# Kernel optimization log

Measured on AMD Instinct MI355X. Metric: run time of the kernel, lower is better.

Reference implementation:

```python
import jax, jax.numpy as jnp
import numpy as np

H = 4096
V = 32000
IGNORE_INDEX = -100
BETA = 0.1
ALPHA = 1.0
LABEL_SMOOTHING = 0.0


def setup_inputs() -> dict:
    key = jax.random.key(0)
    k1, k2, k3 = jax.random.split(key, 3)
    # (2B, T, H): first half chosen, second half rejected
    x = jax.random.normal(k1, (8, 512, H), dtype=jnp.float32)
    y = jax.random.randint(k2, (8, 512), 0, V)
    # LM-head weight, torch Linear layout (V, H)
    W = jax.random.normal(k3, (V, H), dtype=jnp.float32) * 0.02
    return {"x": x, "y": y, "W": W}


def reference(x, y, W):
    # Fused linear + CPO preference loss (math of LigerFusedLinearCPOLoss).
    # logits: (2B, T, V)
    logits = jnp.einsum("bth,vh->btv", x, W)
    logp = jax.nn.log_softmax(logits, axis=-1)

    loss_mask = (y != IGNORE_INDEX)
    y_safe = jnp.where(loss_mask, y, 0)
    # per-token target log-prob: (2B, T)
    tok_lp = jnp.take_along_axis(logp, y_safe[..., None], axis=-1)[..., 0]
    maskf = loss_mask.astype(logp.dtype)

    # per-sequence average log-prob over non-ignored tokens: (2B,)
    avg_lp = (tok_lp * maskf).sum(-1) / maskf.sum(-1)

    B2 = x.shape[0]
    B = B2 // 2
    chosen_logps = avg_lp[:B]
    rejected_logps = avg_lp[B:]

    # CPO preference term (simple sigmoid loss with label smoothing)
    d = BETA * (chosen_logps - rejected_logps)
    pref_loss = (
        -jax.nn.log_sigmoid(d) * (1.0 - LABEL_SMOOTHING)
        - jax.nn.log_sigmoid(-d) * LABEL_SMOOTHING
    ).sum() / B

    # NLL term on the chosen half, normalized by chosen non-ignored token count
    nll = -(tok_lp[:B] * maskf[:B]).sum() / maskf[:B].sum()

    return ALPHA * nll + pref_loss
```

## Files before the change

kernel.cpp:

```cpp
#include <hip/hip_runtime.h>
#include <hip/hip_bf16.h>

#define H_DIM 4096
#define M_TOK 4096
#define V_DIM 32000
#define BM 128
#define BN 128
#define BK 64

typedef unsigned short ushort_t;
typedef __attribute__((ext_vector_type(8))) short short8;
typedef __attribute__((ext_vector_type(4))) float f32x4;

__device__ __forceinline__ unsigned short f2bf(float f) {
    unsigned int u = __float_as_uint(f);
    u += 0x7FFFu + ((u >> 16) & 1u);
    return (unsigned short)(u >> 16);
}

__device__ __forceinline__ void gl2lds16(const void* g, void* l) {
    __builtin_amdgcn_global_load_lds(
        (const __attribute__((address_space(1))) unsigned int*)g,
        (__attribute__((address_space(3))) unsigned int*)l, 16, 0, 0);
}

__global__ void cast_f32_bf16(const float* __restrict__ src,
                              ushort_t* __restrict__ dst, size_t n) {
    size_t i = ((size_t)blockIdx.x * 256 + threadIdx.x) * 8;
    if (i >= n) return;
    float4 a = *(const float4*)(src + i);
    float4 b = *(const float4*)(src + i + 4);
    short8 p = { (short)f2bf(a.x), (short)f2bf(a.y), (short)f2bf(a.z), (short)f2bf(a.w),
                 (short)f2bf(b.x), (short)f2bf(b.y), (short)f2bf(b.z), (short)f2bf(b.w) };
    *(short8*)(dst + i) = p;
}

template <bool WPRE>
__global__ __launch_bounds__(256) void gemm_fused(
    const ushort_t* __restrict__ xb,
    const ushort_t* __restrict__ wb,
    const float*    __restrict__ wf,
    const int*      __restrict__ y,
    float* __restrict__ sums,
    float* __restrict__ label)
{
    int i = blockIdx.x;
    int xcd = i & 7;
    int j = i >> 3;
    int nouter = j >> 5;
    int mt = j & 31;
    int ntile = xcd + 8 * nouter;
    if (ntile >= 250) return;
    int m0 = mt * BM;
    int n0 = ntile * BN;

    __shared__ ushort_t lA[BM * BK];
    __shared__ ushort_t lB[BN * BK];

    int t = threadIdx.x;
    int lane = t & 63;
    int wid = t >> 6;
    int wm = (wid >> 1) * 64;
    int wn = (wid & 1) * 64;
    int lrow = lane & 15;
    int lko = (lane >> 4) * 8;
    int sw = (lane & 7) * 8;

    f32x4 acc[4][4] = {};

    int csw = ((t & 7) ^ ((t >> 3) & 7)) * 8;
    const ushort_t* ag = xb + (size_t)(m0 + (t >> 3)) * H_DIM + csw;
    ushort_t* al = &lA[t * 8];
    const ushort_t* bg = WPRE ? (wb + (size_t)(n0 + (t >> 3)) * H_DIM + csw) : (const ushort_t*)0;
    ushort_t* bl = &lB[t * 8];
    const float* wg = WPRE ? (const float*)0 : (wf + (size_t)(n0 + (t >> 1)) * H_DIM + (t & 1) * 32);
    int wrow = t >> 1;

    for (int kt = 0; kt < H_DIM; kt += BK) {
        #pragma unroll
        for (int r = 0; r < 4; r++)
            gl2lds16(ag + kt + (size_t)r * 32 * H_DIM, al + r * 2048);
        if (WPRE) {
            #pragma unroll
            for (int r = 0; r < 4; r++)
                gl2lds16(bg + kt + (size_t)r * 32 * H_DIM, bl + r * 2048);
        } else {
            #pragma unroll
            for (int q = 0; q < 4; q++) {
                float4 v0 = *(const float4*)(wg + kt + 8 * q);
                float4 v1 = *(const float4*)(wg + kt + 8 * q + 4);
                short8 p = { (short)f2bf(v0.x), (short)f2bf(v0.y), (short)f2bf(v0.z), (short)f2bf(v0.w),
                             (short)f2bf(v1.x), (short)f2bf(v1.y), (short)f2bf(v1.z), (short)f2bf(v1.w) };
                int e = (t & 1) * 32 + 8 * q;
                *(short8*)(&lB[wrow * BK + (e ^ ((wrow & 7) * 8))]) = p;
            }
        }
        __syncthreads();
        #pragma unroll
        for (int kk = 0; kk < BK; kk += 32) {
            short8 af[4], bfr[4];
            #pragma unroll
            for (int mi = 0; mi < 4; mi++)
                af[mi] = *(const short8*)&lA[(wm + mi * 16 + lrow) * BK + ((kk + lko) ^ sw)];
            #pragma unroll
            for (int ni = 0; ni < 4; ni++)
                bfr[ni] = *(const short8*)&lB[(wn + ni * 16 + lrow) * BK + ((kk + lko) ^ sw)];
            #pragma unroll
            for (int mi = 0; mi < 4; mi++)
                #pragma unroll
                for (int ni = 0; ni < 4; ni++)
                    acc[mi][ni] = __builtin_amdgcn_mfma_f32_16x16x32_bf16(
                        af[mi], bfr[ni], acc[mi][ni], 0, 0, 0);
        }
        __syncthreads();
    }

    int quad = lane >> 4;
    #pragma unroll
    for (int mi = 0; mi < 4; mi++) {
        #pragma unroll
        for (int ii = 0; ii < 4; ii++) {
            int row = wm + mi * 16 + quad * 4 + ii;
            int gm = m0 + row;
            int yv = y[gm];
            int c = yv - n0 - wn;
            #pragma unroll
            for (int ni = 0; ni < 4; ni++) {
                if (c == ni * 16 + lrow) label[gm] = acc[mi][ni][ii];
            }
            float s = __expf(acc[mi][0][ii]) + __expf(acc[mi][1][ii]) +
                      __expf(acc[mi][2][ii]) + __expf(acc[mi][3][ii]);
            s += __shfl_xor(s, 1);
            s += __shfl_xor(s, 2);
            s += __shfl_xor(s, 4);
            s += __shfl_xor(s, 8);
            if (lrow == 0) atomicAdd(&sums[gm], s);
        }
    }
}

__global__ void finalize_loss(const float* __restrict__ sums,
                              const float* __restrict__ label,
                              const int* __restrict__ y,
                              float* __restrict__ out) {
    __shared__ float red[512];
    __shared__ float redc[512];
    __shared__ float s_lp[8], s_cnt[8];
    int t = threadIdx.x;
    for (int s = 0; s < 8; s++) {
        int idx = s * 512 + t;
        int yv = y[idx];
        float maskf = (yv != -100) ? 1.0f : 0.0f;
        float lp = (label[idx] - logf(sums[idx])) * maskf;
        red[t] = lp;
        redc[t] = maskf;
        __syncthreads();
        for (int off = 256; off > 0; off >>= 1) {
            if (t < off) { red[t] += red[t + off]; redc[t] += redc[t + off]; }
            __syncthreads();
        }
        if (t == 0) { s_lp[s] = red[0]; s_cnt[s] = redc[0]; }
        __syncthreads();
    }
    if (t == 0) {
        float pref = 0.0f, nll_num = 0.0f, nll_den = 0.0f;
        for (int b = 0; b < 4; b++) {
            float avgc = s_lp[b] / s_cnt[b];
            float avgr = s_lp[b + 4] / s_cnt[b + 4];
            float d = 0.1f * (avgc - avgr);
            float ls = fminf(d, 0.0f) - log1pf(expf(-fabsf(d)));
            pref += -ls;
            nll_num += s_lp[b];
            nll_den += s_cnt[b];
        }
        pref *= 0.25f;
        float nll = -nll_num / nll_den;
        out[0] = nll + pref;
    }
}

extern "C" void kernel_launch(void* const* d_in, const int* in_sizes, int n_in,
                              void* d_out, int out_size, void* d_ws, size_t ws_size,
                              hipStream_t stream) {
    const float* x = (const float*)d_in[0];
    const int*   y = (const int*)d_in[1];
    const float* W = (const float*)d_in[2];
    float* out = (float*)d_out;

    char* ws = (char*)d_ws;
    ushort_t* xb   = (ushort_t*)ws;
    float* sums    = (float*)(ws + 33554432);
    float* label   = (float*)(ws + 33554432 + 16384);
    ushort_t* Wb   = (ushort_t*)(ws + 33587200);
    bool wpre = ws_size >= 295731200ull;

    hipMemsetAsync(sums, 0, 32768, stream);

    cast_f32_bf16<<<8192, 256, 0, stream>>>(x, xb, (size_t)16777216);
    if (wpre) {
        cast_f32_bf16<<<64000, 256, 0, stream>>>(W, Wb, (size_t)131072000);
        gemm_fused<true><<<8192, 256, 0, stream>>>(xb, Wb, (const float*)0, y, sums, label);
    } else {
        gemm_fused<false><<<8192, 256, 0, stream>>>(xb, (const ushort_t*)0, W, y, sums, label);
    }
    finalize_loss<<<1, 512, 0, stream>>>(sums, label, y, out);
}
```

Baseline: 2.269 ms.

## Add 256x256 double-buffered 8-wave GEMM with interleaved loads and MFMA

```diff
diff --git a/kernel.cpp b/kernel.cpp
--- a/kernel.cpp
+++ b/kernel.cpp
@@ -4,9 +4,6 @@
 #define H_DIM 4096
 #define M_TOK 4096
 #define V_DIM 32000
-#define BM 128
-#define BN 128
-#define BK 64
 
 typedef unsigned short ushort_t;
 typedef __attribute__((ext_vector_type(8))) short short8;
@@ -35,10 +32,148 @@
     *(short8*)(dst + i) = p;
 }
 
-template <bool WPRE>
-__global__ __launch_bounds__(256) void gemm_fused(
+__global__ __launch_bounds__(512, 2) void gemm_fused8(
     const ushort_t* __restrict__ xb,
     const ushort_t* __restrict__ wb,
+    const int*      __restrict__ y,
+    float* __restrict__ sums,
+    float* __restrict__ label)
+{
+    int i = blockIdx.x;
+    int g = (i & 7) * 250 + (i >> 3);
+    int mtile = g & 15;
+    int ntile = g >> 4;
+    int m0 = mtile * 256;
+    int n0 = ntile * 256;
+
+    __shared__ ushort_t lA[2][256 * 64];
+    __shared__ ushort_t lB[2][256 * 64];
+
+    int t = threadIdx.x;
+    int lane = t & 63;
+    int wid = t >> 6;
+    int wm = (wid >> 2) * 128;
+    int wn = (wid & 3) * 64;
+    int lrow = lane & 15;
+    int lko = (lane >> 4) * 8;
+    int sw = (lane & 7) * 8;
+
+    int sr = t >> 3;
+    int strow = (sr & 31) + (sr >> 5) * 64;
+    int cswel = ((t & 7) ^ (sr & 7)) * 8;
+    int ch8 = (t & 7) * 8;
+    const ushort_t* agb = xb + (size_t)m0 * H_DIM + cswel;
+    const ushort_t* bgb = wb + (size_t)n0 * H_DIM + cswel;
+
+#define ST_A(BUF, RB, KT) gl2lds16(agb + (size_t)((RB) + sr) * H_DIM + (KT), \
+                                   &lA[BUF][((RB) + sr) * 64 + ch8])
+#define ST_B(BUF, SB, KT) gl2lds16(bgb + (size_t)((SB) + strow) * H_DIM + (KT), \
+                                   &lB[BUF][((SB) + strow) * 64 + ch8])
+
+#define RD_A(C, QM) \
+    _Pragma("unroll") for (int mi2 = 0; mi2 < 4; mi2++) { \
+        af[mi2][0] = *(const short8*)&lA[C][(wm + (QM) * 64 + mi2 * 16 + lrow) * 64 + (lko ^ sw)]; \
+        af[mi2][1] = *(const short8*)&lA[C][(wm + (QM) * 64 + mi2 * 16 + lrow) * 64 + ((32 + lko) ^ sw)]; \
+    }
+#define RD_B(C, QN) do { \
+        bf[0][0] = *(const short8*)&lB[C][(wn + (QN) * 32 + lrow) * 64 + (lko ^ sw)]; \
+        bf[0][1] = *(const short8*)&lB[C][(wn + (QN) * 32 + lrow) * 64 + ((32 + lko) ^ sw)]; \
+        bf[1][0] = *(const short8*)&lB[C][(wn + (QN) * 32 + 16 + lrow) * 64 + (lko ^ sw)]; \
+        bf[1][1] = *(const short8*)&lB[C][(wn + (QN) * 32 + 16 + lrow) * 64 + ((32 + lko) ^ sw)]; \
+    } while (0)
+
+#define MFMA16(QM, N0) \
+    __builtin_amdgcn_s_setprio(1); \
+    _Pragma("unroll") for (int mi2 = 0; mi2 < 4; mi2++) { \
+        acc[(QM)*4+mi2][(N0)]   = __builtin_amdgcn_mfma_f32_16x16x32_bf16(af[mi2][0], bf[0][0], acc[(QM)*4+mi2][(N0)],   0, 0, 0); \
+        acc[(QM)*4+mi2][(N0)]   = __builtin_amdgcn_mfma_f32_16x16x32_bf16(af[mi2][1], bf[0][1], acc[(QM)*4+mi2][(N0)],   0, 0, 0); \
+        acc[(QM)*4+mi2][(N0)+1] = __builtin_amdgcn_mfma_f32_16x16x32_bf16(af[mi2][0], bf[1][0], acc[(QM)*4+mi2][(N0)+1], 0, 0, 0); \
+        acc[(QM)*4+mi2][(N0)+1] = __builtin_amdgcn_mfma_f32_16x16x32_bf16(af[mi2][1], bf[1][1], acc[(QM)*4+mi2][(N0)+1], 0, 0, 0); \
+    } \
+    __builtin_amdgcn_s_setprio(0);
+
+#define VM4 asm volatile("s_waitcnt vmcnt(4)" ::: "memory")
+#define VM2 asm volatile("s_waitcnt vmcnt(2)" ::: "memory")
+#define VM0 asm volatile("s_waitcnt vmcnt(0)" ::: "memory")
+#define BAR __builtin_amdgcn_s_barrier()
+
+#define TILE_BODY(C, NC, KT1, KT2, DO01, DO23, W0, W1, W2, W3) do { \
+     \
+    if (DO01) { ST_A(NC, 64, KT1); ST_A(NC, 192, KT1); } \
+    W0; BAR; \
+    RD_A(C, 0); RD_B(C, 0); \
+    MFMA16(0, 0); \
+    BAR; \
+     \
+    if (DO01) { ST_B(NC, 0, KT1); ST_B(NC, 128, KT1); } \
+    W1; BAR; \
+    RD_B(C, 1); \
+    MFMA16(0, 2); \
+    BAR; \
+     \
+    if (DO23) { ST_A(C, 0, KT2); ST_A(C, 128, KT2); } \
+    W2; BAR; \
+    RD_A(C, 1); \
+    MFMA16(1, 2); \
+    BAR; \
+     \
+    if (DO23) { ST_B(C, 32, KT2); ST_B(C, 160, KT2); } \
+    W3; BAR; \
+    RD_B(C, 0); \
+    MFMA16(1, 0); \
+    BAR; \
+} while (0)
+
+    f32x4 acc[8][4] = {};
+    short8 af[4][2], bf[2][2];
+
+    ST_A(0, 0, 0);   ST_A(0, 128, 0);
+    ST_B(0, 32, 0);  ST_B(0, 160, 0);
+    ST_A(0, 64, 0);  ST_A(0, 192, 0);
+    ST_B(0, 0, 0);   ST_B(0, 128, 0);
+    ST_A(1, 0, 64);  ST_A(1, 128, 64);
+    ST_B(1, 32, 64); ST_B(1, 160, 64);
+    VM4;
+    BAR;
+
+    int c = 0;
+    for (int tt = 0; tt < 62; tt++) {
+        TILE_BODY(c, c ^ 1, (tt + 1) * 64, (tt + 2) * 64, 1, 1, VM4, VM4, VM4, VM4);
+        c ^= 1;
+    }
+    TILE_BODY(c, c ^ 1, 63 * 64, 0, 1, 0, VM4, VM4, VM2, VM0);
+    c ^= 1;
+    TILE_BODY(c, c, 0, 0, 0, 0, (void)0, (void)0, (void)0, (void)0);
+
+    int quad = lane >> 4;
+    #pragma unroll
+    for (int ai = 0; ai < 8; ai++) {
+        #pragma unroll
+        for (int ii = 0; ii < 4; ii++) {
+            int row = wm + (ai >> 2) * 64 + (ai & 3) * 16 + quad * 4 + ii;
+            int gm = m0 + row;
+            int yv = y[gm];
+            int cc = yv - n0 - wn;
+            #pragma unroll
+            for (int ni = 0; ni < 4; ni++) {
+                if (cc == ni * 16 + lrow) label[gm] = acc[ai][ni][ii];
+            }
+            float s = __expf(acc[ai][0][ii]) + __expf(acc[ai][1][ii]) +
+                      __expf(acc[ai][2][ii]) + __expf(acc[ai][3][ii]);
+            s += __shfl_xor(s, 1);
+            s += __shfl_xor(s, 2);
+            s += __shfl_xor(s, 4);
+            s += __shfl_xor(s, 8);
+            if (lrow == 0) atomicAdd(&sums[gm], s);
+        }
+    }
+}
+
+#define BM 128
+#define BN 128
+#define BK 64
+__global__ __launch_bounds__(256) void gemm_fused_f32(
+    const ushort_t* __restrict__ xb,
     const float*    __restrict__ wf,
     const int*      __restrict__ y,
     float* __restrict__ sums,
@@ -71,29 +206,21 @@
     int csw = ((t & 7) ^ ((t >> 3) & 7)) * 8;
     const ushort_t* ag = xb + (size_t)(m0 + (t >> 3)) * H_DIM + csw;
     ushort_t* al = &lA[t * 8];
-    const ushort_t* bg = WPRE ? (wb + (size_t)(n0 + (t >> 3)) * H_DIM + csw) : (const ushort_t*)0;
-    ushort_t* bl = &lB[t * 8];
-    const float* wg = WPRE ? (const float*)0 : (wf + (size_t)(n0 + (t >> 1)) * H_DIM + (t & 1) * 32);
+    const float* wg = wf + (size_t)(n0 + (t >> 1)) * H_DIM + (t & 1) * 32;
     int wrow = t >> 1;
 
     for (int kt = 0; kt < H_DIM; kt += BK) {
         #pragma unroll
         for (int r = 0; r < 4; r++)
             gl2lds16(ag + kt + (size_t)r * 32 * H_DIM, al + r * 2048);
-        if (WPRE) {
-            #pragma unroll
-            for (int r = 0; r < 4; r++)
-                gl2lds16(bg + kt + (size_t)r * 32 * H_DIM, bl + r * 2048);
-        } else {
-            #pragma unroll
-            for (int q = 0; q < 4; q++) {
-                float4 v0 = *(const float4*)(wg + kt + 8 * q);
-                float4 v1 = *(const float4*)(wg + kt + 8 * q + 4);
-                short8 p = { (short)f2bf(v0.x), (short)f2bf(v0.y), (short)f2bf(v0.z), (short)f2bf(v0.w),
-                             (short)f2bf(v1.x), (short)f2bf(v1.y), (short)f2bf(v1.z), (short)f2bf(v1.w) };
-                int e = (t & 1) * 32 + 8 * q;
-                *(short8*)(&lB[wrow * BK + (e ^ ((wrow & 7) * 8))]) = p;
-            }
+        #pragma unroll
+        for (int q = 0; q < 4; q++) {
+            float4 v0 = *(const float4*)(wg + kt + 8 * q);
+            float4 v1 = *(const float4*)(wg + kt + 8 * q + 4);
+            short8 p = { (short)f2bf(v0.x), (short)f2bf(v0.y), (short)f2bf(v0.z), (short)f2bf(v0.w),
+                         (short)f2bf(v1.x), (short)f2bf(v1.y), (short)f2bf(v1.z), (short)f2bf(v1.w) };
+            int e = (t & 1) * 32 + 8 * q;
+            *(short8*)(&lB[wrow * BK + (e ^ ((wrow & 7) * 8))]) = p;
         }
         __syncthreads();
         #pragma unroll
@@ -123,10 +250,10 @@
             int row = wm + mi * 16 + quad * 4 + ii;
             int gm = m0 + row;
             int yv = y[gm];
-            int c = yv - n0 - wn;
+            int cc = yv - n0 - wn;
             #pragma unroll
             for (int ni = 0; ni < 4; ni++) {
-                if (c == ni * 16 + lrow) label[gm] = acc[mi][ni][ii];
+                if (cc == ni * 16 + lrow) label[gm] = acc[mi][ni][ii];
             }
             float s = __expf(acc[mi][0][ii]) + __expf(acc[mi][1][ii]) +
                       __expf(acc[mi][2][ii]) + __expf(acc[mi][3][ii]);
@@ -199,9 +326,9 @@
     cast_f32_bf16<<<8192, 256, 0, stream>>>(x, xb, (size_t)16777216);
     if (wpre) {
         cast_f32_bf16<<<64000, 256, 0, stream>>>(W, Wb, (size_t)131072000);
-        gemm_fused<true><<<8192, 256, 0, stream>>>(xb, Wb, (const float*)0, y, sums, label);
+        gemm_fused8<<<2000, 512, 0, stream>>>(xb, Wb, y, sums, label);
     } else {
-        gemm_fused<false><<<8192, 256, 0, stream>>>(xb, (const ushort_t*)0, W, y, sums, label);
+        gemm_fused_f32<<<8192, 256, 0, stream>>>(xb, W, y, sums, label);
     }
     finalize_loss<<<1, 512, 0, stream>>>(sums, label, y, out);
 }
```

New measurement: 2.507 ms. +10.5%, slower.
